# Kernel tuning notes

Measured on AMD Instinct MI355X. Metric: run time of the kernel, lower is better.

## Reference

```python
import jax, jax.numpy as jnp
import numpy as np

NCH, NBASIS, NXS, NF = 8, 30, 256, 200
NX = NXS * NXS * 2  # flattened real-pair k-space length


def _fft2c(z):
    # centered orthonormal 2D FFT over the last two axes
    z = jnp.fft.ifftshift(z, axes=(-2, -1))
    z = jnp.fft.fft2(z, norm='ortho')
    return jnp.fft.fftshift(z, axes=(-2, -1))


def setup_inputs() -> dict:
    key = jax.random.key(0)
    k1, k2, k3, k4 = jax.random.split(key, 4)
    x = jax.random.normal(k1, (NBASIS, NXS, NXS, 2), dtype=jnp.float32)
    csmT = jax.random.normal(k2, (NCH, NXS, NXS, 2), dtype=jnp.float32)
    VT = jax.random.normal(k3, (NBASIS, NF), dtype=jnp.float32)
    maskT = jax.random.randint(k4, (NF, NX), 0, 2).astype(jnp.bool_)
    return {"x": x, "csmT": csmT, "VT": VT, "maskT": maskT}


def reference(x, csmT, VT, maskT):
    # x: (nbasis, nx, nx, 2) real-pair complex; csmT: (nch, nx, nx, 2)
    xc = jax.lax.complex(x[..., 0], x[..., 1])          # (b, nx, nx)
    cc = jax.lax.complex(csmT[..., 0], csmT[..., 1])    # (c, nx, nx)
    # coil-sensitivity weighting + centered FFT, batched over all coils/basis
    Y = _fft2c(xc[None, :, :, :] * cc[:, None, :, :])   # (c, b, nx, nx) complex
    # interleave real/imag to match torch reshape of (..., nx, nx, 2) -> (..., NX)
    Yr = jnp.stack([Y.real, Y.imag], axis=-1).reshape(NCH, NBASIS, NX)
    # per-frame subspace projection then mask (mask commutes with the b-sum)
    out = maskT[None, :, :].astype(Yr.dtype) * jnp.einsum('cbn,bf->cfn', Yr, VT)
    return out  # (nch, NF, NX)
```

## Files before the change

kernel.cpp:

```cpp
#include <hip/hip_runtime.h>

#define NCH    8
#define NBASIS 30
#define NXS    256
#define NF     200
#define NX     (NXS*NXS*2)
#define NIMG   (NCH*NBASIS)
#define NFT    13
#define CPB    4

typedef float    f32x4  __attribute__((ext_vector_type(4)));
typedef unsigned u32x4  __attribute__((ext_vector_type(4)));
typedef short    bf16x8 __attribute__((ext_vector_type(8)));

__device__ __forceinline__ int bitrev8(int v) {
    return (int)(__builtin_bitreverse32((unsigned)v) >> 24);
}

__device__ __forceinline__ unsigned short f2bf(float f) {
    unsigned u = __float_as_uint(f);
    return (unsigned short)((u + 0x7FFFu + ((u >> 16) & 1u)) >> 16);
}

__global__ __launch_bounds__(256) void fft_rows_kernel(
        const float* __restrict__ x, const float* __restrict__ csm,
        unsigned short* __restrict__ Amid) {
    __shared__ float ldsRe[4][256];
    __shared__ float ldsIm[4][256];
    __shared__ float twRe[128], twIm[128];

    const int tid   = threadIdx.x;
    const int slice = tid >> 6;
    const int lane  = tid & 63;
    const int blk   = blockIdx.x;
    const int m     = blk >> 6;
    const int row   = ((blk & 63) << 2) + slice;
    const int c     = m / NBASIS;
    const int b     = m - c * NBASIS;

    if (tid < 128) {
        float a = (float)tid * (1.0f / 128.0f);
        twRe[tid] =  cospif(a);
        twIm[tid] = -sinpif(a);
    }

    const float* xr = x   + ((size_t)(b * NXS + row) * NXS) * 2;
    const float* cr = csm + ((size_t)(c * NXS + row) * NXS) * 2;
    #pragma unroll
    for (int j = 0; j < 4; ++j) {
        int col = lane + 64 * j;
        float2 xv = *(const float2*)(xr + col * 2);
        float2 cv = *(const float2*)(cr + col * 2);
        float s = ((row + col) & 1) ? -1.0f : 1.0f;
        ldsRe[slice][col] = s * (xv.x * cv.x - xv.y * cv.y);
        ldsIm[slice][col] = s * (xv.x * cv.y + xv.y * cv.x);
    }
    __syncthreads();

    #pragma unroll
    for (int half = 128; half >= 1; half >>= 1) {
        #pragma unroll
        for (int qq = 0; qq < 2; ++qq) {
            int q  = lane + 64 * qq;
            int g  = q / half;
            int j  = q - g * half;
            int i0 = g * 2 * half + j;
            int i1 = i0 + half;
            float ar = ldsRe[slice][i0], ai = ldsIm[slice][i0];
            float br = ldsRe[slice][i1], bi = ldsIm[slice][i1];
            ldsRe[slice][i0] = ar + br;
            ldsIm[slice][i0] = ai + bi;
            float dr = ar - br, di = ai - bi;
            int k = j * (128 / half);
            float wr = twRe[k], wi = twIm[k];
            ldsRe[slice][i1] = dr * wr - di * wi;
            ldsIm[slice][i1] = dr * wi + di * wr;
        }
        __syncthreads();
    }

    unsigned short* outp = Amid + (size_t)m * NX + (size_t)row * NXS * 2;
    #pragma unroll
    for (int j = 0; j < 4; ++j) {
        int k  = lane + 64 * j;
        int rk = bitrev8(k);
        unsigned pack = (unsigned)f2bf(ldsRe[slice][rk])
                      | ((unsigned)f2bf(ldsIm[slice][rk]) << 16);
        *(unsigned*)(outp + k * 2) = pack;
    }
}

#define CTILE 16
__global__ __launch_bounds__(256) void fft_cols_kernel(
        const unsigned short* __restrict__ Amid, unsigned short* __restrict__ Abf) {
    __shared__ float ldsRe[CTILE][257];
    __shared__ float ldsIm[CTILE][257];
    __shared__ float twRe[128], twIm[128];

    const int tid = threadIdx.x;
    const int blk = blockIdx.x;
    const int m   = blk >> 4;
    const int k0  = (blk & 15) * CTILE;

    if (tid < 128) {
        float a = (float)tid * (1.0f / 128.0f);
        twRe[tid] =  cospif(a);
        twIm[tid] = -sinpif(a);
    }

    const unsigned short* base = Amid + (size_t)m * NX;
    #pragma unroll
    for (int it = 0; it < 16; ++it) {
        int li = it * 256 + tid;
        int r  = li >> 4;
        int cc = li & 15;
        unsigned v = *(const unsigned*)(base + ((size_t)r * NXS + k0 + cc) * 2);
        ldsRe[cc][r] = __uint_as_float(v << 16);
        ldsIm[cc][r] = __uint_as_float(v & 0xFFFF0000u);
    }
    __syncthreads();

    const int slice = tid >> 6;
    const int lane  = tid & 63;

    #pragma unroll
    for (int half = 128; half >= 1; half >>= 1) {
        #pragma unroll
        for (int ci = 0; ci < 4; ++ci) {
            int col = slice * 4 + ci;
            #pragma unroll
            for (int qq = 0; qq < 2; ++qq) {
                int q  = lane + 64 * qq;
                int g  = q / half;
                int j  = q - g * half;
                int i0 = g * 2 * half + j;
                int i1 = i0 + half;
                float ar = ldsRe[col][i0], ai = ldsIm[col][i0];
                float br = ldsRe[col][i1], bi = ldsIm[col][i1];
                ldsRe[col][i0] = ar + br;
                ldsIm[col][i0] = ai + bi;
                float dr = ar - br, di = ai - bi;
                int k = j * (128 / half);
                float wr = twRe[k], wi = twIm[k];
                ldsRe[col][i1] = dr * wr - di * wi;
                ldsIm[col][i1] = dr * wi + di * wr;
            }
        }
        __syncthreads();
    }

    unsigned short* obase = Abf + (size_t)m * NX;
    #pragma unroll
    for (int it = 0; it < 16; ++it) {
        int li = it * 256 + tid;
        int ky = li >> 4;
        int cc = li & 15;
        int kx = k0 + cc;
        int rk = bitrev8(ky);
        float s = (((ky + kx) & 1) ? -1.0f : 1.0f) * (1.0f / 256.0f);
        unsigned pack = ((unsigned)f2bf(s * ldsIm[cc][rk]) << 16)
                      |  (unsigned)f2bf(s * ldsRe[cc][rk]);
        *(unsigned*)(obase + ((size_t)ky * NXS + kx) * 2) = pack;
    }
}

__global__ __launch_bounds__(256) void vt_prep_kernel(
        const float* __restrict__ VT, unsigned short* __restrict__ VTfrag) {
    int i = blockIdx.x * 256 + threadIdx.x;
    if (i >= NFT * 512) return;
    int ft = i >> 9, r = i & 511, lane = r >> 3, j = r & 7;
    int k = (lane >> 4) * 8 + j;
    int f = ft * 16 + (lane & 15);
    unsigned short v = 0;
    if (k < NBASIS && f < NF) v = f2bf(VT[k * NF + f]);
    VTfrag[i] = v;
}

__global__ __launch_bounds__(256) void project_mfma_kernel(
        const unsigned short* __restrict__ Abf,
        const unsigned short* __restrict__ VTfrag,
        const void*           __restrict__ maskT,
        float* __restrict__ out) {
    __shared__ __align__(16) unsigned char smem[4][4864];
    __shared__ __align__(16) unsigned short vtlds[NFT * 512];

    const int tid  = threadIdx.x;
    const int wv   = tid >> 6;
    const int lane = tid & 63;
    const int ksec = lane >> 4;
    const int fr   = lane & 15;
    const int c0   = blockIdx.y * CPB;
    const int n0w  = blockIdx.x * 256 + wv * 64;

    {
        const u32x4* src = (const u32x4*)VTfrag;
        u32x4*       dst = (u32x4*)vtlds;
        for (int i = tid; i < NFT * 512 / 8; i += 256) dst[i] = src[i];
    }

    const unsigned* mwd = (const unsigned*)maskT;
    bool byteMode = false;
    #pragma unroll
    for (int i = 0; i < 32; ++i) byteMode |= (mwd[i] > 1u);

    unsigned mbits[7] = {0u, 0u, 0u, 0u, 0u, 0u, 0u};
    if (byteMode) {
        const unsigned char* mb = (const unsigned char*)maskT + n0w + ksec * 4;
        #pragma unroll
        for (int ft = 0; ft < NFT; ++ft) {
            const int f_l = ft * 16 + fr;
            #pragma unroll
            for (int fn = 0; fn < 4; ++fn) {
                unsigned w = (f_l < NF)
                    ? *(const unsigned*)(mb + (size_t)f_l * NX + fn * 16) : 0u;
                unsigned nib = (w | (w >> 7) | (w >> 14) | (w >> 21)) & 0xFu;
                const int p = ft * 16 + fn * 4;
                mbits[p >> 5] |= nib << (p & 31);
            }
        }
    } else {
        const int* mi = (const int*)maskT + n0w + ksec * 4;
        #pragma unroll
        for (int ft = 0; ft < NFT; ++ft) {
            const int f_l = ft * 16 + fr;
            #pragma unroll
            for (int fn = 0; fn < 4; ++fn) {
                unsigned nib = 0u;
                if (f_l < NF) {
                    u32x4 v = *(const u32x4*)(mi + (size_t)f_l * NX + fn * 16);
                    nib = (v.x ? 1u : 0u) | (v.y ? 2u : 0u)
                        | (v.z ? 4u : 0u) | (v.w ? 8u : 0u);
                }
                const int p = ft * 16 + fn * 4;
                mbits[p >> 5] |= nib << (p & 31);
            }
        }
    }

    unsigned short (*ylds)[72] = (unsigned short (*)[72])smem[wv];
    float          (*ldsW)[68] = (float (*)[68])smem[wv];

    __syncthreads();

    #pragma unroll 1
    for (int cc = 0; cc < CPB; ++cc) {
        const int c = c0 + cc;

        {
            const unsigned short* src = Abf + (size_t)c * NBASIS * NX + n0w;
            #pragma unroll
            for (int i = 0; i < 4; ++i) {
                int idx = lane + 64 * i;
                int row = idx >> 3, seg = idx & 7;
                u32x4 v = (u32x4)(0u, 0u, 0u, 0u);
                if (row < NBASIS)
                    v = *(const u32x4*)(src + (size_t)row * NX + seg * 8);
                *(u32x4*)&ylds[row][seg * 8] = v;
            }
        }
        __builtin_amdgcn_wave_barrier();
        asm volatile("s_waitcnt lgkmcnt(0)" ::: "memory");
        __builtin_amdgcn_sched_barrier(0);

        bf16x8 yfrag[4];
        #pragma unroll
        for (int fn = 0; fn < 4; ++fn) {
            #pragma unroll
            for (int j = 0; j < 8; ++j)
                yfrag[fn][j] = (short)ylds[ksec * 8 + j][fn * 16 + fr];
        }
        __builtin_amdgcn_wave_barrier();
        asm volatile("s_waitcnt lgkmcnt(0)" ::: "memory");
        __builtin_amdgcn_sched_barrier(0);

        float* outc = out + (size_t)c * NF * NX;

        #pragma unroll
        for (int ft = 0; ft < NFT; ++ft) {
            bf16x8 vt = *(const bf16x8*)&vtlds[ft * 512 + lane * 8];

            #pragma unroll
            for (int fn = 0; fn < 4; ++fn) {
                const int p = ft * 16 + fn * 4;
                const unsigned nib = (mbits[p >> 5] >> (p & 31)) & 0xFu;
                f32x4 d = __builtin_amdgcn_mfma_f32_16x16x32_bf16(
                    yfrag[fn], vt, (f32x4)(0.f, 0.f, 0.f, 0.f), 0, 0, 0);
                f32x4 o;
                #pragma unroll
                for (int r = 0; r < 4; ++r)
                    o[r] = (nib & (1u << r)) ? d[r] : 0.0f;
                *(f32x4*)&ldsW[fr][fn * 16 + ksec * 4] = o;
            }
            __builtin_amdgcn_wave_barrier();
            asm volatile("s_waitcnt lgkmcnt(0)" ::: "memory");
            __builtin_amdgcn_sched_barrier(0);

            #pragma unroll
            for (int rl = 0; rl < 4; ++rl) {
                int f_local = rl * 4 + ksec;
                int f = ft * 16 + f_local;
                f32x4 v = *(const f32x4*)&ldsW[f_local][fr * 4];
                if (f < NF)
                    __builtin_nontemporal_store(v,
                        (f32x4*)(outc + (size_t)f * NX + n0w + fr * 4));
            }
            __builtin_amdgcn_wave_barrier();
        }
    }
}

extern "C" void kernel_launch(void* const* d_in, const int* in_sizes, int n_in,
                              void* d_out, int out_size, void* d_ws, size_t ws_size,
                              hipStream_t stream) {
    const float* x    = (const float*)d_in[0];
    const float* csm  = (const float*)d_in[1];
    const float* VT   = (const float*)d_in[2];
    const void*  mask = d_in[3];
    float* out = (float*)d_out;

    char* ws = (char*)d_ws;
    unsigned short* Amid   = (unsigned short*)ws;
    unsigned short* Abf    = (unsigned short*)(ws + ((size_t)64 << 20));
    unsigned short* VTfrag = (unsigned short*)(ws + ((size_t)128 << 20));

    vt_prep_kernel<<<(NFT * 512 + 255) / 256, 256, 0, stream>>>(VT, VTfrag);
    fft_rows_kernel<<<NIMG * 64, 256, 0, stream>>>(x, csm, Amid);
    fft_cols_kernel<<<NIMG * 16, 256, 0, stream>>>(Amid, Abf);
    project_mfma_kernel<<<dim3(NX / 256, NCH / CPB), 256, 0, stream>>>(
        Abf, VTfrag, mask, out);
}
```

Measured before the change: 327.0 us.

## Widen projection tile per wave, drop channel loop, hold VT fragments in registers

Each wave in the projection kernel now covers 256 k-space columns for a single coil instead of 64 columns looped over 4 coils, with one block per coil. VT fragments are kept in registers rather than LDS, and mask bits for the wider tile are packed into 26 registers. LDS staging uses XOR swizzling to reduce bank conflicts, and a block barrier per frame tile paces the waves. The aim is to amortise the mask and VT loads over more output and lengthen contiguous stores, at the cost of much higher register pressure (capped at 2 waves/EU) and mask reads that are no longer shared across coils.

```diff
diff --git a/kernel.cpp b/kernel.cpp
--- a/kernel.cpp
+++ b/kernel.cpp
@@ -7,7 +7,6 @@
 #define NX     (NXS*NXS*2)
 #define NIMG   (NCH*NBASIS)
 #define NFT    13
-#define CPB    4
 
 typedef float    f32x4  __attribute__((ext_vector_type(4)));
 typedef unsigned u32x4  __attribute__((ext_vector_type(4)));
@@ -176,136 +175,140 @@
     VTfrag[i] = v;
 }
 
-__global__ __launch_bounds__(256) void project_mfma_kernel(
+__global__ __launch_bounds__(256)
+__attribute__((amdgpu_waves_per_eu(2, 2)))
+void project_mfma_kernel(
         const unsigned short* __restrict__ Abf,
         const unsigned short* __restrict__ VTfrag,
         const void*           __restrict__ maskT,
         float* __restrict__ out) {
-    __shared__ __align__(16) unsigned char smem[4][4864];
-    __shared__ __align__(16) unsigned short vtlds[NFT * 512];
+    __shared__ __align__(16) unsigned char smem[4][16384];
 
     const int tid  = threadIdx.x;
     const int wv   = tid >> 6;
     const int lane = tid & 63;
     const int ksec = lane >> 4;
     const int fr   = lane & 15;
-    const int c0   = blockIdx.y * CPB;
-    const int n0w  = blockIdx.x * 256 + wv * 64;
-
-    {
-        const u32x4* src = (const u32x4*)VTfrag;
-        u32x4*       dst = (u32x4*)vtlds;
-        for (int i = tid; i < NFT * 512 / 8; i += 256) dst[i] = src[i];
-    }
+    const int c    = blockIdx.y;
+    const int n0w  = blockIdx.x * 1024 + wv * 256;
+
+    unsigned char* myLds = smem[wv];
+
+    bf16x8 vtreg[NFT];
+    #pragma unroll
+    for (int ft = 0; ft < NFT; ++ft)
+        vtreg[ft] = *(const bf16x8*)(VTfrag + ft * 512 + lane * 8);
 
     const unsigned* mwd = (const unsigned*)maskT;
     bool byteMode = false;
     #pragma unroll
     for (int i = 0; i < 32; ++i) byteMode |= (mwd[i] > 1u);
 
-    unsigned mbits[7] = {0u, 0u, 0u, 0u, 0u, 0u, 0u};
+    unsigned mbits[NFT * 2];
+    #pragma unroll
+    for (int i = 0; i < NFT * 2; ++i) mbits[i] = 0u;
     if (byteMode) {
         const unsigned char* mb = (const unsigned char*)maskT + n0w + ksec * 4;
         #pragma unroll
         for (int ft = 0; ft < NFT; ++ft) {
-            const int f_l = ft * 16 + fr;
+            const int  f_l = ft * 16 + fr;
+            const bool fok = f_l < NF;
             #pragma unroll
-            for (int fn = 0; fn < 4; ++fn) {
-                unsigned w = (f_l < NF)
+            for (int fn = 0; fn < 16; ++fn) {
+                unsigned w = fok
                     ? *(const unsigned*)(mb + (size_t)f_l * NX + fn * 16) : 0u;
                 unsigned nib = (w | (w >> 7) | (w >> 14) | (w >> 21)) & 0xFu;
-                const int p = ft * 16 + fn * 4;
-                mbits[p >> 5] |= nib << (p & 31);
+                mbits[ft * 2 + (fn >> 3)] |= nib << ((fn & 7) * 4);
             }
         }
     } else {
         const int* mi = (const int*)maskT + n0w + ksec * 4;
         #pragma unroll
         for (int ft = 0; ft < NFT; ++ft) {
-            const int f_l = ft * 16 + fr;
+            const int  f_l = ft * 16 + fr;
+            const bool fok = f_l < NF;
             #pragma unroll
-            for (int fn = 0; fn < 4; ++fn) {
+            for (int fn = 0; fn < 16; ++fn) {
                 unsigned nib = 0u;
-                if (f_l < NF) {
+                if (fok) {
                     u32x4 v = *(const u32x4*)(mi + (size_t)f_l * NX + fn * 16);
                     nib = (v.x ? 1u : 0u) | (v.y ? 2u : 0u)
                         | (v.z ? 4u : 0u) | (v.w ? 8u : 0u);
                 }
-                const int p = ft * 16 + fn * 4;
-                mbits[p >> 5] |= nib << (p & 31);
+                mbits[ft * 2 + (fn >> 3)] |= nib << ((fn & 7) * 4);
             }
         }
     }
 
-    unsigned short (*ylds)[72] = (unsigned short (*)[72])smem[wv];
-    float          (*ldsW)[68] = (float (*)[68])smem[wv];
-
-    __syncthreads();
-
-    #pragma unroll 1
-    for (int cc = 0; cc < CPB; ++cc) {
-        const int c = c0 + cc;
-
-        {
-            const unsigned short* src = Abf + (size_t)c * NBASIS * NX + n0w;
+    {
+        const unsigned short* src = Abf + (size_t)c * NBASIS * NX + n0w;
+        #pragma unroll
+        for (int i = 0; i < 15; ++i) {
+            int flat = i * 64 + lane;
+            int row  = flat >> 5, seg = flat & 31;
+            u32x4 v = *(const u32x4*)(src + (size_t)row * NX + seg * 8);
+            int blk = (seg ^ (row & 7) ^ ((row >> 3) << 2)) & 31;
+            *(u32x4*)(myLds + row * 512 + blk * 16) = v;
+        }
+        int row = 30 + (lane >> 5), seg = lane & 31;
+        int blk = (seg ^ (row & 7) ^ ((row >> 3) << 2)) & 31;
+        *(u32x4*)(myLds + row * 512 + blk * 16) = (u32x4)(0u, 0u, 0u, 0u);
+    }
+    asm volatile("s_waitcnt lgkmcnt(0)" ::: "memory");
+    __builtin_amdgcn_sched_barrier(0);
+
+    bf16x8 yfrag[16];
+    #pragma unroll
+    for (int fn = 0; fn < 16; ++fn) {
+        #pragma unroll
+        for (int j = 0; j < 8; ++j) {
+            int col = fn * 16 + fr;
+            int row = ksec * 8 + j;
+            int blk = ((col >> 3) ^ j ^ (ksec << 2)) & 31;
+            unsigned short v = *(const unsigned short*)
+                (myLds + row * 512 + blk * 16 + (col & 7) * 2);
+            yfrag[fn][j] = (short)v;
+        }
+    }
+    asm volatile("s_waitcnt lgkmcnt(0)" ::: "memory");
+    __builtin_amdgcn_sched_barrier(0);
+
+    float* outc = out + (size_t)c * NF * NX;
+
+    #pragma unroll
+    for (int ft = 0; ft < NFT; ++ft) {
+        __builtin_amdgcn_s_barrier();
+
+        bf16x8 vt = vtreg[ft];
+        #pragma unroll
+        for (int fn = 0; fn < 16; ++fn) {
+            unsigned nib = (mbits[ft * 2 + (fn >> 3)] >> ((fn & 7) * 4)) & 0xFu;
+            f32x4 d = __builtin_amdgcn_mfma_f32_16x16x32_bf16(
+                yfrag[fn], vt, (f32x4)(0.f, 0.f, 0.f, 0.f), 0, 0, 0);
+            f32x4 o;
             #pragma unroll
-            for (int i = 0; i < 4; ++i) {
-                int idx = lane + 64 * i;
-                int row = idx >> 3, seg = idx & 7;
-                u32x4 v = (u32x4)(0u, 0u, 0u, 0u);
-                if (row < NBASIS)
-                    v = *(const u32x4*)(src + (size_t)row * NX + seg * 8);
-                *(u32x4*)&ylds[row][seg * 8] = v;
-            }
-        }
-        __builtin_amdgcn_wave_barrier();
+            for (int r = 0; r < 4; ++r)
+                o[r] = (nib & (1u << r)) ? d[r] : 0.0f;
+            int blkw = ((fn * 4 + ksec) ^ (fr & 7)) & 63;
+            *(f32x4*)(myLds + fr * 1024 + blkw * 16) = o;
+        }
         asm volatile("s_waitcnt lgkmcnt(0)" ::: "memory");
         __builtin_amdgcn_sched_barrier(0);
-
-        bf16x8 yfrag[4];
-        #pragma unroll
-        for (int fn = 0; fn < 4; ++fn) {
-            #pragma unroll
-            for (int j = 0; j < 8; ++j)
-                yfrag[fn][j] = (short)ylds[ksec * 8 + j][fn * 16 + fr];
-        }
         __builtin_amdgcn_wave_barrier();
+
+        #pragma unroll
+        for (int fl = 0; fl < 16; ++fl) {
+            int f = ft * 16 + fl;
+            if (f < NF) {
+                int blkr = (lane ^ (fl & 7)) & 63;
+                f32x4 v = *(const f32x4*)(myLds + fl * 1024 + blkr * 16);
+                __builtin_nontemporal_store(v,
+                    (f32x4*)(outc + (size_t)f * NX + n0w + lane * 4));
+            }
+        }
         asm volatile("s_waitcnt lgkmcnt(0)" ::: "memory");
         __builtin_amdgcn_sched_barrier(0);
-
-        float* outc = out + (size_t)c * NF * NX;
-
-        #pragma unroll
-        for (int ft = 0; ft < NFT; ++ft) {
-            bf16x8 vt = *(const bf16x8*)&vtlds[ft * 512 + lane * 8];
-
-            #pragma unroll
-            for (int fn = 0; fn < 4; ++fn) {
-                const int p = ft * 16 + fn * 4;
-                const unsigned nib = (mbits[p >> 5] >> (p & 31)) & 0xFu;
-                f32x4 d = __builtin_amdgcn_mfma_f32_16x16x32_bf16(
-                    yfrag[fn], vt, (f32x4)(0.f, 0.f, 0.f, 0.f), 0, 0, 0);
-                f32x4 o;
-                #pragma unroll
-                for (int r = 0; r < 4; ++r)
-                    o[r] = (nib & (1u << r)) ? d[r] : 0.0f;
-                *(f32x4*)&ldsW[fr][fn * 16 + ksec * 4] = o;
-            }
-            __builtin_amdgcn_wave_barrier();
-            asm volatile("s_waitcnt lgkmcnt(0)" ::: "memory");
-            __builtin_amdgcn_sched_barrier(0);
-
-            #pragma unroll
-            for (int rl = 0; rl < 4; ++rl) {
-                int f_local = rl * 4 + ksec;
-                int f = ft * 16 + f_local;
-                f32x4 v = *(const f32x4*)&ldsW[f_local][fr * 4];
-                if (f < NF)
-                    __builtin_nontemporal_store(v,
-                        (f32x4*)(outc + (size_t)f * NX + n0w + fr * 4));
-            }
-            __builtin_amdgcn_wave_barrier();
-        }
+        __builtin_amdgcn_wave_barrier();
     }
 }
 
@@ -326,6 +329,6 @@
     vt_prep_kernel<<<(NFT * 512 + 255) / 256, 256, 0, stream>>>(VT, VTfrag);
     fft_rows_kernel<<<NIMG * 64, 256, 0, stream>>>(x, csm, Amid);
     fft_cols_kernel<<<NIMG * 16, 256, 0, stream>>>(Amid, Abf);
-    project_mfma_kernel<<<dim3(NX / 256, NCH / CPB), 256, 0, stream>>>(
+    project_mfma_kernel<<<dim3(NX / 1024, NCH), 256, 0, stream>>>(
         Abf, VTfrag, mask, out);
 }
```

Result: slower. 786.6 us (+140.6%).
